# Optimization experiments

Measured on AMD Instinct MI355X. Metric: run time of the kernel, lower is better.

The kernel has to match this reference:

```python
import jax, jax.numpy as jnp
import numpy as np

UP = 4  # bilinear upsample factor (mask_h*4, mask_w*4)

def setup_inputs() -> dict:
    key = jax.random.key(0)
    k1, k2, k3 = jax.random.split(key, 3)
    B, N, NM, H, W, D = 4, 8400, 32, 160, 160, 100
    mc = jax.random.normal(k1, (B, N, NM), dtype=jnp.float32)
    proto = jax.random.normal(k2, (B, NM, H, W), dtype=jnp.float32)
    det_indices = jax.random.randint(k3, (B, D), 0, N, dtype=jnp.int64)
    return {"mc": mc, "proto": proto, "det_indices": det_indices}

def reference(mc, proto, det_indices):
    # mc: [B, N, nm]; proto: [B, nm, H, W]; det_indices: [B, D]
    B, NM, H, W = proto.shape
    D = det_indices.shape[1]
    bs_idx = jnp.arange(B)[:, None]                       # [B, 1]
    selected_mc = mc[bs_idx, det_indices]                 # [B, D, nm] gather
    det_masks = jax.nn.sigmoid(
        jnp.einsum('bdn,bnhw->bdhw', selected_mc, proto)  # [B, D, H, W]
    )
    # torch F.interpolate(mode='bilinear', align_corners=False) == half-pixel bilinear
    up = jax.image.resize(det_masks, (B, D, H * UP, W * UP), method='bilinear')
    return (up > 0.5).astype(jnp.uint8)                   # [B, D, 4H, 4W]
```

## Files before the change

kernel.cpp:

```cpp
#include <hip/hip_runtime.h>
#include <math.h>

#define BQ   4
#define NQ   8400
#define NMQ  32
#define HQ   160
#define WQ   160
#define DQ   100
#define TH   16
#define THALO (TH + 2)
#define OH   (TH * 4)
#define OW   (WQ * 4)

__device__ __forceinline__ float cephes_expf(float x) {
    float m = floorf(fmaf(x, 1.44269504088896341f, 0.5f));
    float r = fmaf(m, -0.693359375f, x);
    r = fmaf(m, 2.12194440e-4f, r);
    float r2 = __fmul_rn(r, r);
    float y = 1.9875691500E-4f;
    y = fmaf(y, r, 1.3981999507E-3f);
    y = fmaf(y, r, 8.3334519073E-3f);
    y = fmaf(y, r, 4.1665795894E-2f);
    y = fmaf(y, r, 1.6666665459E-1f);
    y = fmaf(y, r, 5.0000001201E-1f);
    y = fmaf(y, r2, r);
    y = __fadd_rn(y, 1.0f);
    int im = (int)m;
    float s = __int_as_float((im + 127) << 23);
    return __fmul_rn(y, s);
}

__global__ __launch_bounds__(256) void seg_kernel(
    const float* __restrict__ mc,
    const float* __restrict__ proto,
    const int*   __restrict__ det,
    int*         __restrict__ out)
{
    __shared__ float tile[THALO][WQ];
    __shared__ float mcs[NMQ];

    const int tid = threadIdx.x;
    const int rt  = blockIdx.x;
    const int d   = blockIdx.y;
    const int b   = blockIdx.z;
    const int r0  = rt * TH;

    if (tid < NMQ) {
        int idx = det[b * DQ + d];
        mcs[tid] = mc[((size_t)b * NQ + (size_t)idx) * NMQ + tid];
    }
    __syncthreads();

    const float* pb = proto + (size_t)b * NMQ * HQ * WQ;
    for (int p = tid; p < THALO * WQ; p += 256) {
        int h = p / WQ;
        int w = p - h * WQ;
        int gh = r0 - 1 + h;
        gh = gh < 0 ? 0 : (gh > HQ - 1 ? HQ - 1 : gh);
        const float* pp = pb + gh * WQ + w;
        float acc = 0.0f;
        #pragma unroll
        for (int n = 0; n < NMQ; ++n) {
            acc = fmaf(pp[(size_t)n * HQ * WQ], mcs[n], acc);
        }
        float e = cephes_expf(-acc);
        tile[h][w] = 1.0f / __fadd_rn(1.0f, e);
    }
    __syncthreads();

    const float FYB[4] = {0.625f, 0.875f, 0.125f, 0.375f};
    const float FYT[4] = {0.375f, 0.125f, 0.875f, 0.625f};

    int* ob = out + ((size_t)b * DQ + d) * ((size_t)OW * HQ * 4)
                  + (size_t)r0 * 4 * OW;

    for (int g = tid; g < OH * WQ; g += 256) {
        int oyl = g / WQ;
        int oxg = g - oyl * WQ;
        int phase = oyl & 3;
        int iy = (oyl >> 2) + (phase >> 1);
        int goy = r0 * 4 + oyl;
        bool yedge = (goy < 2) || (goy >= 4 * HQ - 2);

        int cm = (oxg == 0)      ? 0      : oxg - 1;
        int cp = (oxg == WQ - 1) ? WQ - 1 : oxg + 1;

        float tm = tile[iy][cm],     t0 = tile[iy][oxg],     tp = tile[iy][cp];
        float bm = tile[iy + 1][cm], b0 = tile[iy + 1][oxg], bp = tile[iy + 1][cp];

        float Tm, T0, Tp;
        if (yedge) {
            Tm = tm; T0 = t0; Tp = tp;
        } else {
            float wt = FYT[phase], wb = FYB[phase];
            Tm = fmaf(wb, bm, __fmul_rn(wt, tm));
            T0 = fmaf(wb, b0, __fmul_rn(wt, t0));
            Tp = fmaf(wb, bp, __fmul_rn(wt, tp));
        }

        float v0, v1, v2, v3;
        if (oxg == 0) {
            v0 = T0; v1 = T0;
        } else {
            v0 = fmaf(0.625f, T0, __fmul_rn(0.375f, Tm));
            v1 = fmaf(0.875f, T0, __fmul_rn(0.125f, Tm));
        }
        if (oxg == WQ - 1) {
            v2 = T0; v3 = T0;
        } else {
            v2 = fmaf(0.125f, Tp, __fmul_rn(0.875f, T0));
            v3 = fmaf(0.375f, Tp, __fmul_rn(0.625f, T0));
        }

        int4 r;
        r.x = v0 > 0.5f ? 1 : 0;
        r.y = v1 > 0.5f ? 1 : 0;
        r.z = v2 > 0.5f ? 1 : 0;
        r.w = v3 > 0.5f ? 1 : 0;

        *(int4*)(ob + (size_t)oyl * OW + (size_t)oxg * 4) = r;
    }
}

extern "C" void kernel_launch(void* const* d_in, const int* in_sizes, int n_in,
                              void* d_out, int out_size, void* d_ws, size_t ws_size,
                              hipStream_t stream) {
    const float* mc    = (const float*)d_in[0];
    const float* proto = (const float*)d_in[1];
    const int*   det   = (const int*)d_in[2];
    int* out = (int*)d_out;

    dim3 grid(HQ / TH, DQ, BQ);
    seg_kernel<<<grid, 256, 0, stream>>>(mc, proto, det, out);
}
```

Before: 690.4 us.

## Split into low-res mask GEMM kernel and separate upsample kernel via workspace

Replaces the single fused kernel with two kernels when the workspace is large enough. The first computes sigmoid masks at low resolution, each thread reusing its 32 proto values across 20 detections held in registers. The second reads those masks and does the bilinear upsample and threshold with a smaller row tile. This removes the redundant halo recomputation and the repeated proto reads per detection. In exchange it adds a 41 MB intermediate write and read plus a second launch, and falls back to the fused kernel when the workspace is too small.

New measurement: 697.1 us. Within noise of the previous version (+1.0%).

```diff
diff --git a/kernel.cpp b/kernel.cpp
--- a/kernel.cpp
+++ b/kernel.cpp
@@ -7,10 +7,10 @@
 #define HQ   160
 #define WQ   160
 #define DQ   100
-#define TH   16
-#define THALO (TH + 2)
-#define OH   (TH * 4)
+#define HW   (HQ * WQ)
 #define OW   (WQ * 4)
+#define DCH  20
+#define TR   4
 
 __device__ __forceinline__ float cephes_expf(float x) {
     float m = floorf(fmaf(x, 1.44269504088896341f, 0.5f));
@@ -30,7 +30,126 @@
     return __fmul_rn(y, s);
 }
 
-__global__ __launch_bounds__(256) void seg_kernel(
+__global__ __launch_bounds__(256) void lowres_kernel(
+    const float* __restrict__ mc,
+    const float* __restrict__ proto,
+    const int*   __restrict__ det,
+    float*       __restrict__ ws)
+{
+    __shared__ float mcs[DCH][NMQ];
+    const int tid  = threadIdx.x;
+    const int pix  = blockIdx.x * 256 + tid;
+    const int d0   = blockIdx.y * DCH;
+    const int b    = blockIdx.z;
+
+    for (int i = tid; i < DCH * NMQ; i += 256) {
+        int dd = i / NMQ, c = i - dd * NMQ;
+        int idx = det[b * DQ + d0 + dd];
+        mcs[dd][c] = mc[((size_t)b * NQ + (size_t)idx) * NMQ + c];
+    }
+    __syncthreads();
+
+    const float* pb = proto + (size_t)b * NMQ * HW + pix;
+    float p[NMQ];
+    #pragma unroll
+    for (int c = 0; c < NMQ; ++c) p[c] = pb[(size_t)c * HW];
+
+    float acc[DCH];
+    #pragma unroll
+    for (int dd = 0; dd < DCH; ++dd) acc[dd] = 0.0f;
+    #pragma unroll
+    for (int c = 0; c < NMQ; ++c) {
+        #pragma unroll
+        for (int dd = 0; dd < DCH; ++dd)
+            acc[dd] = fmaf(p[c], mcs[dd][c], acc[dd]);
+    }
+
+    float* wb = ws + ((size_t)b * DQ + d0) * HW + pix;
+    #pragma unroll
+    for (int dd = 0; dd < DCH; ++dd) {
+        float e = cephes_expf(-acc[dd]);
+        wb[(size_t)dd * HW] = 1.0f / __fadd_rn(1.0f, e);
+    }
+}
+
+__global__ __launch_bounds__(256) void upsample_kernel(
+    const float* __restrict__ ws,
+    int*         __restrict__ out)
+{
+    __shared__ float tile[TR + 2][WQ];
+    const int tid = threadIdx.x;
+    const int r0  = blockIdx.x * TR;
+    const int d   = blockIdx.y;
+    const int b   = blockIdx.z;
+
+    const float* sb = ws + ((size_t)b * DQ + d) * HW;
+    for (int i = tid; i < (TR + 2) * WQ; i += 256) {
+        int h = i / WQ, w = i - h * WQ;
+        int gh = r0 - 1 + h;
+        gh = gh < 0 ? 0 : (gh > HQ - 1 ? HQ - 1 : gh);
+        tile[h][w] = sb[gh * WQ + w];
+    }
+    __syncthreads();
+
+    const float FYB[4] = {0.625f, 0.875f, 0.125f, 0.375f};
+    const float FYT[4] = {0.375f, 0.125f, 0.875f, 0.625f};
+
+    int* ob = out + ((size_t)b * DQ + d) * ((size_t)HW * 16)
+                  + (size_t)r0 * 4 * OW;
+
+    for (int g = tid; g < TR * 4 * WQ; g += 256) {
+        int oyl = g / WQ;
+        int oxg = g - oyl * WQ;
+        int phase = oyl & 3;
+        int iy = (oyl >> 2) + (phase >> 1);
+        int goy = r0 * 4 + oyl;
+        bool yedge = (goy < 2) || (goy >= 4 * HQ - 2);
+
+        int cm = (oxg == 0)      ? 0      : oxg - 1;
+        int cp = (oxg == WQ - 1) ? WQ - 1 : oxg + 1;
+
+        float tm = tile[iy][cm],     t0 = tile[iy][oxg],     tp = tile[iy][cp];
+        float bm = tile[iy + 1][cm], b0 = tile[iy + 1][oxg], bp = tile[iy + 1][cp];
+
+        float Tm, T0, Tp;
+        if (yedge) {
+            Tm = tm; T0 = t0; Tp = tp;
+        } else {
+            float wt = FYT[phase], wb = FYB[phase];
+            Tm = fmaf(wb, bm, __fmul_rn(wt, tm));
+            T0 = fmaf(wb, b0, __fmul_rn(wt, t0));
+            Tp = fmaf(wb, bp, __fmul_rn(wt, tp));
+        }
+
+        float v0, v1, v2, v3;
+        if (oxg == 0) {
+            v0 = T0; v1 = T0;
+        } else {
+            v0 = fmaf(0.625f, T0, __fmul_rn(0.375f, Tm));
+            v1 = fmaf(0.875f, T0, __fmul_rn(0.125f, Tm));
+        }
+        if (oxg == WQ - 1) {
+            v2 = T0; v3 = T0;
+        } else {
+            v2 = fmaf(0.125f, Tp, __fmul_rn(0.875f, T0));
+            v3 = fmaf(0.375f, Tp, __fmul_rn(0.625f, T0));
+        }
+
+        int4 r;
+        r.x = v0 > 0.5f ? 1 : 0;
+        r.y = v1 > 0.5f ? 1 : 0;
+        r.z = v2 > 0.5f ? 1 : 0;
+        r.w = v3 > 0.5f ? 1 : 0;
+
+        *(int4*)(ob + (size_t)oyl * OW + (size_t)oxg * 4) = r;
+    }
+}
+
+#define TH    16
+#define THALO (TH + 2)
+#define OH    (TH * 4)
+
+__global__ __launch_bounds__(256) void seg_fused_kernel(
     const float* __restrict__ mc,
     const float* __restrict__ proto,
     const int*   __restrict__ det,
@@ -51,7 +170,7 @@
     }
     __syncthreads();
 
-    const float* pb = proto + (size_t)b * NMQ * HQ * WQ;
+    const float* pb = proto + (size_t)b * NMQ * HW;
     for (int p = tid; p < THALO * WQ; p += 256) {
         int h = p / WQ;
         int w = p - h * WQ;
@@ -60,9 +179,8 @@
         const float* pp = pb + gh * WQ + w;
         float acc = 0.0f;
         #pragma unroll
-        for (int n = 0; n < NMQ; ++n) {
-            acc = fmaf(pp[(size_t)n * HQ * WQ], mcs[n], acc);
-        }
+        for (int n = 0; n < NMQ; ++n)
+            acc = fmaf(pp[(size_t)n * HW], mcs[n], acc);
         float e = cephes_expf(-acc);
         tile[h][w] = 1.0f / __fadd_rn(1.0f, e);
     }
@@ -71,7 +189,7 @@
     const float FYB[4] = {0.625f, 0.875f, 0.125f, 0.375f};
     const float FYT[4] = {0.375f, 0.125f, 0.875f, 0.625f};
 
-    int* ob = out + ((size_t)b * DQ + d) * ((size_t)OW * HQ * 4)
+    int* ob = out + ((size_t)b * DQ + d) * ((size_t)HW * 16)
                   + (size_t)r0 * 4 * OW;
 
     for (int g = tid; g < OH * WQ; g += 256) {
@@ -89,9 +207,8 @@
         float bm = tile[iy + 1][cm], b0 = tile[iy + 1][oxg], bp = tile[iy + 1][cp];
 
         float Tm, T0, Tp;
-        if (yedge) {
-            Tm = tm; T0 = t0; Tp = tp;
-        } else {
+        if (yedge) { Tm = tm; T0 = t0; Tp = tp; }
+        else {
             float wt = FYT[phase], wb = FYB[phase];
             Tm = fmaf(wb, bm, __fmul_rn(wt, tm));
             T0 = fmaf(wb, b0, __fmul_rn(wt, t0));
@@ -99,15 +216,13 @@
         }
 
         float v0, v1, v2, v3;
-        if (oxg == 0) {
-            v0 = T0; v1 = T0;
-        } else {
+        if (oxg == 0) { v0 = T0; v1 = T0; }
+        else {
             v0 = fmaf(0.625f, T0, __fmul_rn(0.375f, Tm));
             v1 = fmaf(0.875f, T0, __fmul_rn(0.125f, Tm));
         }
-        if (oxg == WQ - 1) {
-            v2 = T0; v3 = T0;
-        } else {
+        if (oxg == WQ - 1) { v2 = T0; v3 = T0; }
+        else {
             v2 = fmaf(0.125f, Tp, __fmul_rn(0.875f, T0));
             v3 = fmaf(0.375f, Tp, __fmul_rn(0.625f, T0));
         }
@@ -130,6 +245,15 @@
     const int*   det   = (const int*)d_in[2];
     int* out = (int*)d_out;
 
-    dim3 grid(HQ / TH, DQ, BQ);
-    seg_kernel<<<grid, 256, 0, stream>>>(mc, proto, det, out);
-}
+    const size_t need = (size_t)BQ * DQ * HW * sizeof(float);
+    if (ws_size >= need) {
+        float* ws = (float*)d_ws;
+        dim3 g1(HW / 256, DQ / DCH, BQ);
+        lowres_kernel<<<g1, 256, 0, stream>>>(mc, proto, det, ws);
+        dim3 g2(HQ / TR, DQ, BQ);
+        upsample_kernel<<<g2, 256, 0, stream>>>(ws, out);
+    } else {
+        dim3 grid(HQ / TH, DQ, BQ);
+        seg_fused_kernel<<<grid, 256, 0, stream>>>(mc, proto, det, out);
+    }
+}
```

## Split into low-res mask GEMM kernel and separate upsample kernel via workspace

Applied to the files above, without the earlier changes.

The fused kernel is split into two. The first computes sigmoid(mc·proto) for 20 detections per pixel, so each proto load is reused across detections and halo rows are no longer recomputed. The second reads the low-res masks from workspace with vector loads and writes the upsampled thresholded output using nontemporal stores. The cost is an extra ~41 MB workspace write and read, plus a second launch.

After: 679.3 us. Within noise of the previous version (-1.6%).

```diff
diff --git a/kernel.cpp b/kernel.cpp
--- a/kernel.cpp
+++ b/kernel.cpp
@@ -7,10 +7,13 @@
 #define HQ   160
 #define WQ   160
 #define DQ   100
-#define TH   16
-#define THALO (TH + 2)
-#define OH   (TH * 4)
+#define HW   (HQ * WQ)
 #define OW   (WQ * 4)
+#define DCH  20
+#define TR   8
+
+typedef int   ivec4 __attribute__((ext_vector_type(4)));
+typedef float fvec4 __attribute__((ext_vector_type(4)));
 
 __device__ __forceinline__ float cephes_expf(float x) {
     float m = floorf(fmaf(x, 1.44269504088896341f, 0.5f));
@@ -30,51 +33,75 @@
     return __fmul_rn(y, s);
 }
 
-__global__ __launch_bounds__(256) void seg_kernel(
+__global__ __launch_bounds__(256) void lowres_kernel(
     const float* __restrict__ mc,
     const float* __restrict__ proto,
     const int*   __restrict__ det,
-    int*         __restrict__ out)
+    float*       __restrict__ ws)
 {
-    __shared__ float tile[THALO][WQ];
-    __shared__ float mcs[NMQ];
+    __shared__ float mcs[DCH][NMQ];
+    const int tid  = threadIdx.x;
+    const int pix  = blockIdx.x * 256 + tid;
+    const int d0   = blockIdx.y * DCH;
+    const int b    = blockIdx.z;
 
-    const int tid = threadIdx.x;
-    const int rt  = blockIdx.x;
-    const int d   = blockIdx.y;
-    const int b   = blockIdx.z;
-    const int r0  = rt * TH;
-
-    if (tid < NMQ) {
-        int idx = det[b * DQ + d];
-        mcs[tid] = mc[((size_t)b * NQ + (size_t)idx) * NMQ + tid];
+    for (int i = tid; i < DCH * NMQ; i += 256) {
+        int dd = i / NMQ, c = i - dd * NMQ;
+        int idx = det[b * DQ + d0 + dd];
+        mcs[dd][c] = mc[((size_t)b * NQ + (size_t)idx) * NMQ + c];
     }
     __syncthreads();
 
-    const float* pb = proto + (size_t)b * NMQ * HQ * WQ;
-    for (int p = tid; p < THALO * WQ; p += 256) {
-        int h = p / WQ;
-        int w = p - h * WQ;
+    const float* pb = proto + (size_t)b * NMQ * HW + pix;
+    float p[NMQ];
+    #pragma unroll
+    for (int c = 0; c < NMQ; ++c) p[c] = pb[(size_t)c * HW];
+
+    float acc[DCH];
+    #pragma unroll
+    for (int dd = 0; dd < DCH; ++dd) acc[dd] = 0.0f;
+    #pragma unroll
+    for (int c = 0; c < NMQ; ++c) {
+        #pragma unroll
+        for (int dd = 0; dd < DCH; ++dd)
+            acc[dd] = fmaf(p[c], mcs[dd][c], acc[dd]);
+    }
+
+    float* wb = ws + ((size_t)b * DQ + d0) * HW + pix;
+    #pragma unroll
+    for (int dd = 0; dd < DCH; ++dd) {
+        float e = cephes_expf(-acc[dd]);
+        wb[(size_t)dd * HW] = 1.0f / __fadd_rn(1.0f, e);
+    }
+}
+
+__global__ __launch_bounds__(256) void upsample_kernel(
+    const float* __restrict__ ws,
+    int*         __restrict__ out)
+{
+    __shared__ float tile[TR + 2][WQ];
+    const int tid = threadIdx.x;
+    const int r0  = blockIdx.x * TR;
+    const int d   = blockIdx.y;
+    const int b   = blockIdx.z;
+
+    const float* sb = ws + ((size_t)b * DQ + d) * HW;
+    for (int i = tid; i < (TR + 2) * (WQ / 4); i += 256) {
+        int h = i / (WQ / 4), w4 = i - h * (WQ / 4);
         int gh = r0 - 1 + h;
         gh = gh < 0 ? 0 : (gh > HQ - 1 ? HQ - 1 : gh);
-        const float* pp = pb + gh * WQ + w;
-        float acc = 0.0f;
-        #pragma unroll
-        for (int n = 0; n < NMQ; ++n) {
-            acc = fmaf(pp[(size_t)n * HQ * WQ], mcs[n], acc);
-        }
-        float e = cephes_expf(-acc);
-        tile[h][w] = 1.0f / __fadd_rn(1.0f, e);
+        fvec4 v = *(const fvec4*)(sb + gh * WQ + w4 * 4);
+        *(fvec4*)(&tile[h][w4 * 4]) = v;
     }
     __syncthreads();
 
     const float FYB[4] = {0.625f, 0.875f, 0.125f, 0.375f};
     const float FYT[4] = {0.375f, 0.125f, 0.875f, 0.625f};
 
-    int* ob = out + ((size_t)b * DQ + d) * ((size_t)OW * HQ * 4)
+    int* ob = out + ((size_t)b * DQ + d) * ((size_t)HW * 16)
                   + (size_t)r0 * 4 * OW;
 
-    for (int g = tid; g < OH * WQ; g += 256) {
+    for (int g = tid; g < TR * 4 * WQ; g += 256) {
         int oyl = g / WQ;
         int oxg = g - oyl * WQ;
         int phase = oyl & 3;
@@ -112,13 +139,13 @@
             v3 = fmaf(0.375f, Tp, __fmul_rn(0.625f, T0));
         }
 
-        int4 r;
+        ivec4 r;
         r.x = v0 > 0.5f ? 1 : 0;
         r.y = v1 > 0.5f ? 1 : 0;
         r.z = v2 > 0.5f ? 1 : 0;
         r.w = v3 > 0.5f ? 1 : 0;
 
-        *(int4*)(ob + (size_t)oyl * OW + (size_t)oxg * 4) = r;
+        __builtin_nontemporal_store(r, (ivec4*)(ob + (size_t)oyl * OW + (size_t)oxg * 4));
     }
 }
 
@@ -129,7 +156,10 @@
     const float* proto = (const float*)d_in[1];
     const int*   det   = (const int*)d_in[2];
     int* out = (int*)d_out;
+    float* ws = (float*)d_ws;
 
-    dim3 grid(HQ / TH, DQ, BQ);
-    seg_kernel<<<grid, 256, 0, stream>>>(mc, proto, det, out);
+    dim3 g1(HW / 256, DQ / DCH, BQ);
+    lowres_kernel<<<g1, 256, 0, stream>>>(mc, proto, det, ws);
+    dim3 g2(HQ / TR, DQ, BQ);
+    upsample_kernel<<<g2, 256, 0, stream>>>(ws, out);
 }
```
